# Kernel optimization log

Measured on AMD Instinct MI355X. Metric: run time of the kernel, lower is better.

## Reference

```python
import jax, jax.numpy as jnp
import numpy as np

B, W, L = 64, 128, 32   # sentences, words per sentence, max chars per word
V, E, H = 128, 128, 256 # char vocab, char_embedding_size, word_embedding_size


def setup_inputs() -> dict:
    key = jax.random.key(0)
    ks = jax.random.split(key, 14)
    char_ids = jax.random.randint(ks[0], (B, W, L), 0, V, dtype=jnp.int32)
    word_lens = jax.random.randint(ks[1], (B, W), 1, L + 1, dtype=jnp.int32)
    sc = 1.0 / np.sqrt(H)
    n = lambda k, shape, s: (jax.random.normal(k, shape, jnp.float32) * s)
    emb_table = n(ks[2], (V, E), 1.0).at[0].set(0.0)  # padding_idx=0 row is zero
    return {
        "char_ids": char_ids,
        "word_lens": word_lens,
        "emb_table": emb_table,
        "Wih_f": n(ks[3], (4 * H, E), sc), "Whh_f": n(ks[4], (4 * H, H), sc),
        "bih_f": n(ks[5], (4 * H,), sc), "bhh_f": n(ks[6], (4 * H,), sc),
        "Wih_b": n(ks[7], (4 * H, E), sc), "Whh_b": n(ks[8], (4 * H, H), sc),
        "bih_b": n(ks[9], (4 * H,), sc), "bhh_b": n(ks[10], (4 * H,), sc),
        "pW": n(ks[11], (H, 2 * H), 1.0 / np.sqrt(2 * H)),
        "pb": n(ks[12], (H,), 1.0 / np.sqrt(2 * H)),
    }


def _lstm_dir(xW, mask, Whh, reverse):
    # xW: [N, L, 4H] precomputed x@Wih^T + biases; mask: [N, L] bool (t < len).
    # Masked scan: h/c freeze outside valid region, so the final carry is
    # h at t=len-1 (forward) or h at t=0 (backward, reverse=True).
    N = xW.shape[0]
    h0 = jnp.zeros((N, H), xW.dtype)
    c0 = jnp.zeros((N, H), xW.dtype)

    def step(carry, inp):
        h, c = carry
        xw_t, m_t = inp
        g = xw_t + h @ Whh.T                      # [N, 4H]
        i, f, gg, o = jnp.split(g, 4, axis=-1)    # PyTorch gate order i,f,g,o
        c_new = jax.nn.sigmoid(f) * c + jax.nn.sigmoid(i) * jnp.tanh(gg)
        h_new = jax.nn.sigmoid(o) * jnp.tanh(c_new)
        m = m_t[:, None]
        return (jnp.where(m, h_new, h), jnp.where(m, c_new, c)), None

    (h, _), _ = jax.lax.scan(step, (h0, c0),
                             (xW.transpose(1, 0, 2), mask.T), reverse=reverse)
    return h


def reference(char_ids, word_lens, emb_table, Wih_f, Whh_f, bih_f, bhh_f,
              Wih_b, Whh_b, bih_b, bhh_b, pW, pb):
    ids = char_ids.reshape(-1, L)                 # [N, L], N = B*W
    lens = word_lens.reshape(-1)                  # [N]
    x = emb_table[ids]                            # [N, L, E]
    mask = jnp.arange(L)[None, :] < lens[:, None] # [N, L]
    xWf = jnp.einsum('nle,ge->nlg', x, Wih_f) + (bih_f + bhh_f)
    xWb = jnp.einsum('nle,ge->nlg', x, Wih_b) + (bih_b + bhh_b)
    h_fwd = _lstm_dir(xWf, mask, Whh_f, reverse=False)  # fwd dir at last char
    h_bwd = _lstm_dir(xWb, mask, Whh_b, reverse=True)   # bwd dir at first char
    # Original concatenates (backward_at_first, forward_at_last)
    concat = jnp.concatenate([h_bwd, h_fwd], axis=-1)   # [N, 2H]
    wemb = concat @ pW.T + pb                           # [N, H]
    out = wemb.reshape(B, W, H)
    lens_out = jnp.full((B,), W, dtype=jnp.int32)       # words per sentence
    return out, lens_out
```

## Files before the change

kernel.cpp:

```cpp
#include <hip/hip_runtime.h>
#include <hip/hip_bf16.h>
#include <hip/hip_fp8.h>
#include <math.h>

#define B_  64
#define W_  128
#define L_  32
#define V_  128
#define E_  128
#define H_  256
#define G4_ 1024
#define NW  8192
#define KS_ 8
#define ROWB 264
#define HROW 264
#define M_  32

typedef long i64;
typedef short s8v  __attribute__((ext_vector_type(8)));
typedef float f4v  __attribute__((ext_vector_type(4)));

static __device__ __forceinline__ float b2f(unsigned short u) {
  return __uint_as_float(((unsigned int)u) << 16);
}
static __device__ __forceinline__ unsigned char f2fp8(float f) {
  __hip_fp8_e4m3 t(f);
  return (unsigned char)t.__x;
}
static __device__ __forceinline__ float sigm(float x) {
  return __builtin_amdgcn_rcpf(1.f + __expf(-x));
}
static __device__ __forceinline__ float tanh_(float x) {
  return __builtin_amdgcn_rcpf(1.f + __expf(-2.f * x)) * 2.f - 1.f;
}

#define NCHUNK 32
#define CHSZ  (NW / NCHUNK)
__global__ __launch_bounds__(1024) void k_prep(
    const int* __restrict__ word_lens,
    const float* __restrict__ emb,
    const float* __restrict__ Wih_f, const float* __restrict__ bih_f, const float* __restrict__ bhh_f,
    const float* __restrict__ Wih_b, const float* __restrict__ bih_b, const float* __restrict__ bhh_b,
    const float* __restrict__ Whh_f, const float* __restrict__ Whh_b,
    unsigned short* __restrict__ ep4, int* __restrict__ perm,
    unsigned char* __restrict__ Bpack) {
  const int bb  = blockIdx.x;
  const int tid = threadIdx.x;

  if (bb < 256) {
    int v   = bb & (V_ - 1);
    int dir = bb >> 7;
    const float* Wih = dir ? Wih_b : Wih_f;
    const float* b1  = dir ? bih_b : bih_f;
    const float* b2  = dir ? bhh_b : bhh_f;
    __shared__ float es[E_];
    if (tid < E_) es[tid] = emb[v * E_ + tid];
    __syncthreads();
    const float* wr = Wih + tid * E_;
    float a = 0.f;
#pragma unroll 4
    for (int k = 0; k < E_; k += 4) {
      float4 w4 = *(const float4*)(wr + k);
      float4 e4 = *(const float4*)(es + k);
      a += w4.x * e4.x + w4.y * e4.y + w4.z * e4.z + w4.w * e4.w;
    }
    int gate = tid >> 8, col = tid & 255;
    union { __hip_bfloat16 b; unsigned short u; } cv;
    cv.b = __float2bfloat16(a + b1[tid] + b2[tid]);
    ep4[((((dir * V_ + v) << 8) + col) << 2) + gate] = cv.u;
  } else if (bb == 256) {
    __shared__ int cnt_s[NCHUNK][33];
    __shared__ int off_s[NCHUNK][33];
    const int ch  = tid >> 5;
    const int ln  = (tid & 31) + 1;
    const int base = ch * CHSZ;
    int c = 0;
    for (int i = 0; i < CHSZ; ++i) c += (word_lens[base + i] == ln);
    cnt_s[ch][ln] = c;
    __syncthreads();
    if (tid == 0) {
      int run = 0;
      for (int l = 32; l >= 1; --l)
        for (int c2 = 0; c2 < NCHUNK; ++c2) { off_s[c2][l] = run; run += cnt_s[c2][l]; }
    }
    __syncthreads();
    int ptr = off_s[ch][ln];
    for (int i = 0; i < CHSZ; ++i) {
      int wi = base + i;
      if (word_lens[wi] == ln) perm[ptr++] = wi;
    }
  } else {
    int tile = (bb - 257) * 16 + (tid >> 6);
    const int lane = tid & 63;
    const int f    = tile & 7;
    const int w    = (tile >> 3) & 7;
    const int ks   = (tile >> 6) % KS_;
    const int dir  = tile / (64 * KS_);
    const float* Whh = dir ? Whh_b : Whh_f;
    const int u  = f >> 1, jj = f & 1;
    const int nt = u * 16 + 2 * w + jj;
    const int n  = nt * 16 + (lane & 15);
    const int k0 = ks * 32 + (lane >> 4) * 8;
    size_t base = ((((size_t)(dir * KS_ + ks) * 8 + w) * 8 + f) * 64 + lane) * 8;
#pragma unroll
    for (int j = 0; j < 8; ++j)
      Bpack[base + j] = f2fp8(Whh[n * H_ + k0 + j]);
  }
}

__global__ __launch_bounds__(512, 4) void k_lstm(
    const int* __restrict__ char_ids, const int* __restrict__ word_lens,
    const int* __restrict__ perm, const unsigned short* __restrict__ ep4,
    const unsigned char* __restrict__ Bpack, unsigned short* __restrict__ hcat) {
  const int tid  = threadIdx.x;
  const int lane = tid & 63;
  const int w    = tid >> 6;
  const int bid  = blockIdx.x;
  const int q    = bid >> 7;
  const int dir  = q & 1;
  const int chunk = (bid < 256) ? (bid & 127) : ((q == 2) ? 511 - bid : 639 - bid);
  const int w0   = chunk * M_;

  __shared__ unsigned char  hL[2][M_][ROWB];
  __shared__ unsigned short hLb[M_][HROW];
  __shared__ int ids_s[M_][L_ + 1];
  __shared__ int len_s[M_];
  __shared__ int pw_s[M_];

  if (tid < M_) {
    int gw = perm[w0 + tid];
    pw_s[tid]  = gw;
    len_s[tid] = word_lens[gw];
  }
  __syncthreads();
  for (int i = tid; i < M_ * L_; i += 512) {
    int qq = i >> 5;
    ids_s[qq][i & 31] = char_ids[pw_s[qq] * L_ + (i & 31)];
  }
  for (int i = tid; i < M_ * ROWB / 4; i += 512) ((unsigned int*)hL[0])[i] = 0u;
  __syncthreads();

  const int mlen = len_s[0];
  unsigned lrp[2];
#pragma unroll
  for (int mt = 0; mt < 2; ++mt) {
    int bw = mt * 16 + ((lane >> 4) << 2);
    lrp[mt] = (unsigned)len_s[bw] | ((unsigned)len_s[bw + 1] << 8) |
              ((unsigned)len_s[bw + 2] << 16) | ((unsigned)len_s[bw + 3] << 24);
  }

  const char* Bb0 = (const char*)Bpack + (size_t)dir * (KS_ * 8 * 8 * 64 * 8)
                    + (size_t)w * (8 * 64 * 8) + (size_t)lane * 8;
  const char* arA = (const char*)&hL[0][lane & 15][0] + ((lane >> 4) << 3);
  const char* arB = arA + M_ * ROWB;
  unsigned char* hwA = &hL[0][0][0];
  unsigned char* hwB = &hL[1][0][0];
  const ushort4* epv = (const ushort4*)ep4 + ((size_t)dir << 15);
  const int p0 = 2 * w * 16 + (lane & 15);
  const int g4 = (lane >> 4) << 2;

  float c_[2][2][4];
#pragma unroll
  for (int jj = 0; jj < 2; ++jj)
#pragma unroll
    for (int mt = 0; mt < 2; ++mt)
#pragma unroll
      for (int r = 0; r < 4; ++r) c_[jj][mt][r] = 0.f;

  for (int t = 0; t < mlen; ++t) {
    const char* ar = (t & 1) ? arB : arA;
    f4v acc[4][2][2];
#pragma unroll
    for (int u = 0; u < 4; ++u)
#pragma unroll
      for (int jj = 0; jj < 2; ++jj)
#pragma unroll
        for (int mt = 0; mt < 2; ++mt) acc[u][jj][mt] = (f4v){0.f, 0.f, 0.f, 0.f};

    const char* bp0 = Bb0;
    const char* bp1 = Bb0 + 2048;
#pragma unroll 1
    for (int ks = 0; ks < KS_; ++ks) {
      i64 af0 = *(const i64*)(ar + ks * 32);
      i64 af1 = *(const i64*)(ar + 16 * ROWB + ks * 32);
      i64 b0 = *(const i64*)(bp0 + 0);
      i64 b1 = *(const i64*)(bp0 + 512);
      i64 b2 = *(const i64*)(bp0 + 1024);
      i64 b3 = *(const i64*)(bp0 + 1536);
      i64 b4 = *(const i64*)(bp1 + 0);
      i64 b5 = *(const i64*)(bp1 + 512);
      i64 b6 = *(const i64*)(bp1 + 1024);
      i64 b7 = *(const i64*)(bp1 + 1536);
      acc[0][0][0] = __builtin_amdgcn_mfma_f32_16x16x32_fp8_fp8(af0, b0, acc[0][0][0], 0, 0, 0);
      acc[0][0][1] = __builtin_amdgcn_mfma_f32_16x16x32_fp8_fp8(af1, b0, acc[0][0][1], 0, 0, 0);
      acc[0][1][0] = __builtin_amdgcn_mfma_f32_16x16x32_fp8_fp8(af0, b1, acc[0][1][0], 0, 0, 0);
      acc[0][1][1] = __builtin_amdgcn_mfma_f32_16x16x32_fp8_fp8(af1, b1, acc[0][1][1], 0, 0, 0);
      acc[1][0][0] = __builtin_amdgcn_mfma_f32_16x16x32_fp8_fp8(af0, b2, acc[1][0][0], 0, 0, 0);
      acc[1][0][1] = __builtin_amdgcn_mfma_f32_16x16x32_fp8_fp8(af1, b2, acc[1][0][1], 0, 0, 0);
      acc[1][1][0] = __builtin_amdgcn_mfma_f32_16x16x32_fp8_fp8(af0, b3, acc[1][1][0], 0, 0, 0);
      acc[1][1][1] = __builtin_amdgcn_mfma_f32_16x16x32_fp8_fp8(af1, b3, acc[1][1][1], 0, 0, 0);
      acc[2][0][0] = __builtin_amdgcn_mfma_f32_16x16x32_fp8_fp8(af0, b4, acc[2][0][0], 0, 0, 0);
      acc[2][0][1] = __builtin_amdgcn_mfma_f32_16x16x32_fp8_fp8(af1, b4, acc[2][0][1], 0, 0, 0);
      acc[2][1][0] = __builtin_amdgcn_mfma_f32_16x16x32_fp8_fp8(af0, b5, acc[2][1][0], 0, 0, 0);
      acc[2][1][1] = __builtin_amdgcn_mfma_f32_16x16x32_fp8_fp8(af1, b5, acc[2][1][1], 0, 0, 0);
      acc[3][0][0] = __builtin_amdgcn_mfma_f32_16x16x32_fp8_fp8(af0, b6, acc[3][0][0], 0, 0, 0);
      acc[3][0][1] = __builtin_amdgcn_mfma_f32_16x16x32_fp8_fp8(af1, b6, acc[3][0][1], 0, 0, 0);
      acc[3][1][0] = __builtin_amdgcn_mfma_f32_16x16x32_fp8_fp8(af0, b7, acc[3][1][0], 0, 0, 0);
      acc[3][1][1] = __builtin_amdgcn_mfma_f32_16x16x32_fp8_fp8(af1, b7, acc[3][1][1], 0, 0, 0);
      bp0 += 32768;
      bp1 += 32768;
    }

    unsigned char* hwb = (t & 1) ? hwA : hwB;
#pragma unroll
    for (int mt = 0; mt < 2; ++mt) {
      ushort4 xc0[4], xc1[4];
      int act = 0, fin = 0;
#pragma unroll
      for (int r = 0; r < 4; ++r) {
        int len = (int)((lrp[mt] >> (8 * r)) & 255u);
        int tt  = dir ? max(len - 1 - t, 0) : t;
        int id  = ids_s[mt * 16 + g4 + r][tt];
        xc0[r] = epv[(id << 8) + p0];
        xc1[r] = epv[(id << 8) + p0 + 16];
        act |= (t < len)      ? (1 << r) : 0;
        fin |= (t == len - 1) ? (1 << r) : 0;
      }
#pragma unroll
      for (int jj = 0; jj < 2; ++jj) {
#pragma unroll
        for (int r = 0; r < 4; ++r) {
          ushort4 xw = jj ? xc1[r] : xc0[r];
          float gi = acc[0][jj][mt][r] + b2f(xw.x);
          float gf = acc[1][jj][mt][r] + b2f(xw.y);
          float gg = acc[2][jj][mt][r] + b2f(xw.z);
          float go = acc[3][jj][mt][r] + b2f(xw.w);
          float cn = sigm(gf) * c_[jj][mt][r] + sigm(gi) * tanh_(gg);
          float hn = sigm(go) * tanh_(cn);
          const int m = mt * 16 + g4 + r;
          const int p = (2 * w + jj) * 16 + (lane & 15);
          if ((act >> r) & 1) {
            c_[jj][mt][r] = cn;
            hwb[m * ROWB + p] = f2fp8(hn);
          }
          if ((fin >> r) & 1) {
            union { __hip_bfloat16 b; unsigned short u; } cv;
            cv.b = __float2bfloat16(hn);
            hLb[m][p] = cv.u;
          }
        }
      }
    }
    __syncthreads();
  }

  const int off = dir ? 0 : H_;
  for (int i = tid; i < M_ * H_ / 8; i += 512) {
    int qq  = i >> 5;
    int pos = (i & 31) << 3;
    s8v v = *(const s8v*)&hLb[qq][pos];
    *(s8v*)&hcat[(size_t)pw_s[qq] * (2 * H_) + off + pos] = v;
  }
}

#define PM_ 16
__global__ __launch_bounds__(256) void k_proj(
    const unsigned short* __restrict__ hcat, const float* __restrict__ pW,
    const float* __restrict__ pb, float* __restrict__ out) {
  const int tid = threadIdx.x;
  const int n0  = blockIdx.x * PM_;
  __shared__ float hs[PM_][2 * H_];
  for (int i = tid; i < PM_ * 2 * H_ / 8; i += 256) {
    s8v v = *(const s8v*)&hcat[(size_t)n0 * 2 * H_ + i * 8];
    float* d = (float*)hs + i * 8;
#pragma unroll
    for (int j = 0; j < 8; ++j) d[j] = b2f((unsigned short)v[j]);
  }
  __syncthreads();

  const float* pwr = pW + tid * (2 * H_);
  float acc[PM_];
#pragma unroll
  for (int m = 0; m < PM_; ++m) acc[m] = 0.f;

#pragma unroll 2
  for (int k = 0; k < 2 * H_; k += 4) {
    float4 w4 = *(const float4*)(pwr + k);
#pragma unroll
    for (int m = 0; m < PM_; ++m) {
      float4 h4 = *(const float4*)(&hs[m][k]);
      acc[m] += w4.x * h4.x + w4.y * h4.y + w4.z * h4.z + w4.w * h4.w;
    }
  }
  const float bias = pb[tid];
#pragma unroll
  for (int m = 0; m < PM_; ++m) out[(n0 + m) * H_ + tid] = acc[m] + bias;

  if (blockIdx.x == 0 && tid < B_) out[NW * H_ + tid] = (float)W_;
}

extern "C" void kernel_launch(void* const* d_in, const int* in_sizes, int n_in,
                              void* d_out, int out_size, void* d_ws, size_t ws_size,
                              hipStream_t stream) {
  const int*   char_ids  = (const int*)  d_in[0];
  const int*   word_lens = (const int*)  d_in[1];
  const float* emb       = (const float*)d_in[2];
  const float* Wih_f     = (const float*)d_in[3];
  const float* Whh_f     = (const float*)d_in[4];
  const float* bih_f     = (const float*)d_in[5];
  const float* bhh_f     = (const float*)d_in[6];
  const float* Wih_b     = (const float*)d_in[7];
  const float* Whh_b     = (const float*)d_in[8];
  const float* bih_b     = (const float*)d_in[9];
  const float* bhh_b     = (const float*)d_in[10];
  const float* pW        = (const float*)d_in[11];
  const float* pb        = (const float*)d_in[12];
  float* out = (float*)d_out;

  const size_t BPACK_BYTES = (size_t)2 * KS_ * 8 * 8 * 64 * 8;
  const size_t EP4_BYTES   = (size_t)2 * V_ * 256 * 4 * 2;
  unsigned char* Bpack = (unsigned char*)d_ws;
  unsigned short* ep4 = (unsigned short*)((char*)d_ws + BPACK_BYTES);
  int* perm = (int*)((char*)d_ws + BPACK_BYTES + EP4_BYTES);
  unsigned short* hcat = (unsigned short*)((char*)d_ws + BPACK_BYTES + EP4_BYTES + NW * sizeof(int));

  k_prep<<<dim3(321), dim3(1024), 0, stream>>>(word_lens, emb,
                                               Wih_f, bih_f, bhh_f,
                                               Wih_b, bih_b, bhh_b,
                                               Whh_f, Whh_b, ep4, perm, Bpack);
  k_lstm<<<dim3(512), dim3(512), 0, stream>>>(char_ids, word_lens, perm, ep4, Bpack, hcat);
  k_proj<<<dim3(NW / PM_), dim3(256), 0, stream>>>(hcat, pW, pb, out);
}
```

Before: 390.7 us.

## Rewrite projection as bf16 MFMA GEMM with prepacked weight layout

The projection kernel drops its scalar fp32 FMA loop and uses bf16 MFMA 16x16x32 instructions. Each block of 512 threads handles 32 words. k_prep gains 16 blocks that convert pW to bf16 and pack it into the MFMA operand layout. This targets the compute cost of the fp32 projection GEMM, in exchange for bf16 rounding of pW and a larger prep launch.

```diff
diff --git a/kernel.cpp b/kernel.cpp
--- a/kernel.cpp
+++ b/kernel.cpp
@@ -15,6 +15,7 @@
 #define ROWB 264
 #define HROW 264
 #define M_  32
+#define PROW 520
 
 typedef long i64;
 typedef short s8v  __attribute__((ext_vector_type(8)));
@@ -26,6 +27,11 @@
 static __device__ __forceinline__ unsigned char f2fp8(float f) {
   __hip_fp8_e4m3 t(f);
   return (unsigned char)t.__x;
+}
+static __device__ __forceinline__ unsigned short f2bfu(float f) {
+  union { __hip_bfloat16 b; unsigned short u; } cv;
+  cv.b = __float2bfloat16(f);
+  return cv.u;
 }
 static __device__ __forceinline__ float sigm(float x) {
   return __builtin_amdgcn_rcpf(1.f + __expf(-x));
@@ -42,8 +48,9 @@
     const float* __restrict__ Wih_f, const float* __restrict__ bih_f, const float* __restrict__ bhh_f,
     const float* __restrict__ Wih_b, const float* __restrict__ bih_b, const float* __restrict__ bhh_b,
     const float* __restrict__ Whh_f, const float* __restrict__ Whh_b,
+    const float* __restrict__ pW,
     unsigned short* __restrict__ ep4, int* __restrict__ perm,
-    unsigned char* __restrict__ Bpack) {
+    unsigned char* __restrict__ Bpack, unsigned short* __restrict__ pWb) {
   const int bb  = blockIdx.x;
   const int tid = threadIdx.x;
 
@@ -65,9 +72,7 @@
       a += w4.x * e4.x + w4.y * e4.y + w4.z * e4.z + w4.w * e4.w;
     }
     int gate = tid >> 8, col = tid & 255;
-    union { __hip_bfloat16 b; unsigned short u; } cv;
-    cv.b = __float2bfloat16(a + b1[tid] + b2[tid]);
-    ep4[((((dir * V_ + v) << 8) + col) << 2) + gate] = cv.u;
+    ep4[((((dir * V_ + v) << 8) + col) << 2) + gate] = f2bfu(a + b1[tid] + b2[tid]);
   } else if (bb == 256) {
     __shared__ int cnt_s[NCHUNK][33];
     __shared__ int off_s[NCHUNK][33];
@@ -89,7 +94,7 @@
       int wi = base + i;
       if (word_lens[wi] == ln) perm[ptr++] = wi;
     }
-  } else {
+  } else if (bb <= 320) {
     int tile = (bb - 257) * 16 + (tid >> 6);
     const int lane = tid & 63;
     const int f    = tile & 7;
@@ -105,6 +110,18 @@
 #pragma unroll
     for (int j = 0; j < 8; ++j)
       Bpack[base + j] = f2fp8(Whh[n * H_ + k0 + j]);
+  } else {
+    int tp = (bb - 321) * 16 + (tid >> 6);
+    const int lane = tid & 63;
+    const int ks = tp >> 4;
+    const int nt = tp & 15;
+    const int w  = nt >> 1, f = nt & 1;
+    const int n  = nt * 16 + (lane & 15);
+    const int k0 = ks * 32 + (lane >> 4) * 8;
+    size_t base = ((((size_t)ks * 8 + w) * 2 + f) * 64 + lane) * 8;
+#pragma unroll
+    for (int j = 0; j < 8; ++j)
+      pWb[base + j] = f2bfu(pW[n * (2 * H_) + k0 + j]);
   }
 }
 
@@ -243,11 +260,7 @@
             c_[jj][mt][r] = cn;
             hwb[m * ROWB + p] = f2fp8(hn);
           }
-          if ((fin >> r) & 1) {
-            union { __hip_bfloat16 b; unsigned short u; } cv;
-            cv.b = __float2bfloat16(hn);
-            hLb[m][p] = cv.u;
-          }
+          if ((fin >> r) & 1) hLb[m][p] = f2bfu(hn);
         }
       }
     }
@@ -263,40 +276,58 @@
   }
 }
 
-#define PM_ 16
-__global__ __launch_bounds__(256) void k_proj(
-    const unsigned short* __restrict__ hcat, const float* __restrict__ pW,
+__global__ __launch_bounds__(512) void k_proj(
+    const unsigned short* __restrict__ hcat, const unsigned short* __restrict__ pWb,
     const float* __restrict__ pb, float* __restrict__ out) {
-  const int tid = threadIdx.x;
-  const int n0  = blockIdx.x * PM_;
-  __shared__ float hs[PM_][2 * H_];
-  for (int i = tid; i < PM_ * 2 * H_ / 8; i += 256) {
-    s8v v = *(const s8v*)&hcat[(size_t)n0 * 2 * H_ + i * 8];
-    float* d = (float*)hs + i * 8;
-#pragma unroll
-    for (int j = 0; j < 8; ++j) d[j] = b2f((unsigned short)v[j]);
+  const int tid  = threadIdx.x;
+  const int lane = tid & 63;
+  const int w    = tid >> 6;
+  const int n0   = blockIdx.x * 32;
+
+  __shared__ unsigned short hs[32][PROW];
+  for (int i = tid; i < 32 * (2 * H_) / 8; i += 512) {
+    int qq  = i >> 6;
+    int pos = (i & 63) << 3;
+    *(s8v*)&hs[qq][pos] = *(const s8v*)&hcat[(size_t)(n0 + qq) * (2 * H_) + pos];
   }
   __syncthreads();
 
-  const float* pwr = pW + tid * (2 * H_);
-  float acc[PM_];
-#pragma unroll
-  for (int m = 0; m < PM_; ++m) acc[m] = 0.f;
+  const char* ar = (const char*)&hs[lane & 15][0] + ((lane >> 4) << 4);
+  const char* bp = (const char*)pWb + (((size_t)w * 2) * 64 + lane) * 16;
+
+  f4v acc[2][2];
+#pragma unroll
+  for (int f = 0; f < 2; ++f)
+#pragma unroll
+    for (int mt = 0; mt < 2; ++mt) acc[f][mt] = (f4v){0.f, 0.f, 0.f, 0.f};
 
 #pragma unroll 2
-  for (int k = 0; k < 2 * H_; k += 4) {
-    float4 w4 = *(const float4*)(pwr + k);
-#pragma unroll
-    for (int m = 0; m < PM_; ++m) {
-      float4 h4 = *(const float4*)(&hs[m][k]);
-      acc[m] += w4.x * h4.x + w4.y * h4.y + w4.z * h4.z + w4.w * h4.w;
-    }
-  }
-  const float bias = pb[tid];
-#pragma unroll
-  for (int m = 0; m < PM_; ++m) out[(n0 + m) * H_ + tid] = acc[m] + bias;
-
-  if (blockIdx.x == 0 && tid < B_) out[NW * H_ + tid] = (float)W_;
+  for (int ks = 0; ks < 16; ++ks) {
+    s8v a0 = *(const s8v*)(ar + ks * 64);
+    s8v a1 = *(const s8v*)(ar + 16 * PROW * 2 + ks * 64);
+    s8v b0 = *(const s8v*)(bp + (size_t)ks * 16384);
+    s8v b1 = *(const s8v*)(bp + (size_t)ks * 16384 + 1024);
+    acc[0][0] = __builtin_amdgcn_mfma_f32_16x16x32_bf16(a0, b0, acc[0][0], 0, 0, 0);
+    acc[0][1] = __builtin_amdgcn_mfma_f32_16x16x32_bf16(a1, b0, acc[0][1], 0, 0, 0);
+    acc[1][0] = __builtin_amdgcn_mfma_f32_16x16x32_bf16(a0, b1, acc[1][0], 0, 0, 0);
+    acc[1][1] = __builtin_amdgcn_mfma_f32_16x16x32_bf16(a1, b1, acc[1][1], 0, 0, 0);
+  }
+
+#pragma unroll
+  for (int f = 0; f < 2; ++f) {
+    const int col = (2 * w + f) * 16 + (lane & 15);
+    const float bias = pb[col];
+#pragma unroll
+    for (int mt = 0; mt < 2; ++mt) {
+#pragma unroll
+      for (int reg = 0; reg < 4; ++reg) {
+        int row = mt * 16 + ((lane >> 4) << 2) + reg;
+        out[(size_t)(n0 + row) * H_ + col] = acc[f][mt][reg] + bias;
+      }
+    }
+  }
+
+  if (blockIdx.x == 0 && tid < B_) out[(size_t)NW * H_ + tid] = (float)W_;
 }
 
 extern "C" void kernel_launch(void* const* d_in, const int* in_sizes, int n_in,
@@ -318,16 +349,19 @@
   float* out = (float*)d_out;
 
   const size_t BPACK_BYTES = (size_t)2 * KS_ * 8 * 8 * 64 * 8;
+  const size_t PWB_BYTES   = (size_t)16 * 8 * 2 * 64 * 8 * 2;
   const size_t EP4_BYTES   = (size_t)2 * V_ * 256 * 4 * 2;
-  unsigned char* Bpack = (unsigned char*)d_ws;
-  unsigned short* ep4 = (unsigned short*)((char*)d_ws + BPACK_BYTES);
-  int* perm = (int*)((char*)d_ws + BPACK_BYTES + EP4_BYTES);
-  unsigned short* hcat = (unsigned short*)((char*)d_ws + BPACK_BYTES + EP4_BYTES + NW * sizeof(int));
-
-  k_prep<<<dim3(321), dim3(1024), 0, stream>>>(word_lens, emb,
+  unsigned char*  Bpack = (unsigned char*)d_ws;
+  unsigned short* pWb   = (unsigned short*)((char*)d_ws + BPACK_BYTES);
+  unsigned short* ep4   = (unsigned short*)((char*)d_ws + BPACK_BYTES + PWB_BYTES);
+  int* perm = (int*)((char*)d_ws + BPACK_BYTES + PWB_BYTES + EP4_BYTES);
+  unsigned short* hcat = (unsigned short*)((char*)d_ws + BPACK_BYTES + PWB_BYTES + EP4_BYTES + NW * sizeof(int));
+
+  k_prep<<<dim3(337), dim3(1024), 0, stream>>>(word_lens, emb,
                                                Wih_f, bih_f, bhh_f,
                                                Wih_b, bih_b, bhh_b,
-                                               Whh_f, Whh_b, ep4, perm, Bpack);
+                                               Whh_f, Whh_b, pW,
+                                               ep4, perm, Bpack, pWb);
   k_lstm<<<dim3(512), dim3(512), 0, stream>>>(char_ids, word_lens, perm, ep4, Bpack, hcat);
-  k_proj<<<dim3(NW / PM_), dim3(256), 0, stream>>>(hcat, pW, pb, out);
-}
+  k_proj<<<dim3(NW / 32), dim3(512), 0, stream>>>(hcat, pWb, pb, out);
+}
```

Result: faster. 332.7 us (-14.8%).
